# Optimization experiments

Measured on AMD Instinct MI355X. Metric: run time of the kernel, lower is better.

## Reference

```python
import jax, jax.numpy as jnp
import numpy as np
import math

D_MODEL = 1024
NHEAD = 16
D_HEAD = D_MODEL // NHEAD
B, S = 2, 2048


def setup_inputs() -> dict:
    key = jax.random.key(0)
    ks = jax.random.split(key, 8)
    scale = 1.0 / math.sqrt(D_MODEL)
    return {
        "q": jax.random.normal(ks[0], (B, S, D_MODEL), jnp.float32),
        "k": jax.random.normal(ks[1], (B, S, D_MODEL), jnp.float32),
        "v": jax.random.normal(ks[2], (B, S, D_MODEL), jnp.float32),
        "mask": jax.random.randint(ks[3], (B, S, S), 0, 2) == 1,
        "w_q": jax.random.normal(ks[4], (D_MODEL, D_MODEL), jnp.float32) * scale,
        "w_k": jax.random.normal(ks[5], (D_MODEL, D_MODEL), jnp.float32) * scale,
        "w_v": jax.random.normal(ks[6], (D_MODEL, D_MODEL), jnp.float32) * scale,
        "w_o": jax.random.normal(ks[7], (D_MODEL, D_MODEL), jnp.float32) * scale,
    }


def reference(q, k, v, mask, w_q, w_k, w_v, w_o):
    # Linear layers (torch Linear: x @ W.T), then the module's view(B, H, -1, d_head),
    # which is a plain reshape (sequence gets folded with heads), NOT a head-transpose.
    qh = (q @ w_q.T).reshape(B, NHEAD, -1, D_HEAD)  # (B,H,S,dh) via raw reshape
    kh = (k @ w_k.T).reshape(B, NHEAD, -1, D_HEAD)
    vh = (v @ w_v.T).reshape(B, NHEAD, -1, D_HEAD)

    u = jnp.einsum("bhqd,bhkd->bhqk", qh, kh) / math.sqrt(D_HEAD)  # (B,H,S,S)
    m = mask[:, None]  # (B,1,S,S)
    u = jnp.where(m, -jnp.inf, u)
    attn = jax.nn.softmax(u, axis=-1)
    attn = jnp.where(m, 0.0, attn)
    out = jnp.einsum("bhqk,bhkd->bhqd", attn, vh)  # (B,H,S,dh)
    out = out.reshape(B, -1, D_MODEL)  # raw reshape back, matching the module
    return out @ w_o.T
```

## Files before the change

kernel.cpp:

```cpp
#include <hip/hip_runtime.h>
#include <hip/hip_bf16.h>
#include <stdint.h>


typedef __attribute__((ext_vector_type(8))) short short8;
typedef __attribute__((ext_vector_type(4))) short s4v;
typedef __attribute__((ext_vector_type(4))) float floatx4;
using bf16 = __hip_bfloat16;

#define QSCALE 0.18033688011112042f

#define MFMA16(a, b, c) __builtin_amdgcn_mfma_f32_16x16x32_bf16(a, b, c, 0, 0, 0)

__device__ __forceinline__ void load_lds16(const bf16* g, bf16* l) {
  __builtin_amdgcn_global_load_lds(
      (const __attribute__((address_space(1))) void*)g,
      (__attribute__((address_space(3))) void*)l, 16, 0, 0);
}

__device__ __forceinline__ float scrub(float x) {
  return (x == x && fabsf(x) < 1e30f) ? x : 0.0f;
}

__device__ __forceinline__ int swz64(int row, int col) {
  return row * 64 + (col ^ ((row & 7) << 3));
}
__device__ __forceinline__ int swz128(int row, int col) {
  return row * 128 + (col ^ ((row & 15) << 3));
}

__global__ void k_detect(const uint16_t* __restrict__ q,
                         const uint16_t* __restrict__ mask,
                         int* __restrict__ flags) {
  __shared__ int f32, cat;
  const int tid = threadIdx.x;
  if (tid == 0) { f32 = 0; cat = 0; }
  __syncthreads();
  int hit = 0;
#pragma unroll
  for (int j = 0; j < 8; j++) {
    const short8 v8 = *(const short8*)(q + ((size_t)tid * 8 + j) * 8);
#pragma unroll
    for (int t = 0; t < 8; t++) {
      const int e = (((unsigned short)v8[t]) >> 7) & 0xFF;
      if (e == 0 || e == 0xFF) hit = 1;
    }
  }
  if (hit) atomicOr(&f32, 1);
  int c = 0;
  {
    const short8 m8 = *(const short8*)(mask + (size_t)tid * 8);
#pragma unroll
    for (int t = 0; t < 8; t++) {
      const uint32_t hw = (unsigned short)m8[t];
      const int i = tid * 8 + t;
      if (hw == 0x3C00u) c |= 4;
      else if (hw == 0x3F80u) c |= (i & 1) ? 2 : 1;
      else if (hw > 1u) c |= 8;
    }
  }
  if (c) atomicOr(&cat, c);
  __syncthreads();
  if (tid == 0) {
    flags[0] = f32;
    const int cc = cat;
    int mode;
    if (cc & 4)      mode = 2;
    else if (cc & 1) mode = 2;
    else if (cc & 2) mode = 3;
    else if (cc & 8) mode = 0;
    else             mode = 1;
    flags[1] = mode;
  }
}

__global__ __launch_bounds__(256) void k_prep(
    const void* __restrict__ qf, const void* __restrict__ kf,
    const void* __restrict__ vf, const void* __restrict__ wqf,
    const void* __restrict__ wkf, const void* __restrict__ wvf,
    const void* __restrict__ wof, const void* __restrict__ maskp,
    bf16* __restrict__ dst, uint32_t* __restrict__ bits,
    const int* __restrict__ flags, int conv) {
  const int f32 = flags[0];
  const size_t t0 = (size_t)blockIdx.x * 256 + threadIdx.x;
  const size_t nthr = (size_t)gridDim.x * 256;
  if (conv) {
    for (size_t c = t0; c < 2097152; c += nthr) {
      const size_t e = c * 8;
      const void* src; size_t off; float sc = 1.0f;
      if (e < 4194304)       { src = qf;  off = e;            sc = QSCALE; }
      else if (e < 8388608)  { src = kf;  off = e - 4194304;  }
      else if (e < 12582912) { src = vf;  off = e - 8388608;  }
      else if (e < 13631488) { src = wqf; off = e - 12582912; }
      else if (e < 14680064) { src = wkf; off = e - 13631488; }
      else if (e < 15728640) { src = wvf; off = e - 14680064; }
      else                   { src = wof; off = e - 15728640; }
      union { short8 v8; bf16 b[8]; } u;
      if (f32) {
        const float4* s4 = (const float4*)src + (off >> 2);
        const float4 f0 = s4[0];
        const float4 f1 = s4[1];
        u.b[0] = __float2bfloat16(f0.x * sc); u.b[1] = __float2bfloat16(f0.y * sc);
        u.b[2] = __float2bfloat16(f0.z * sc); u.b[3] = __float2bfloat16(f0.w * sc);
        u.b[4] = __float2bfloat16(f1.x * sc); u.b[5] = __float2bfloat16(f1.y * sc);
        u.b[6] = __float2bfloat16(f1.z * sc); u.b[7] = __float2bfloat16(f1.w * sc);
      } else {
        u.v8 = *(const short8*)((const bf16*)src + off);
        if (sc != 1.0f) {
#pragma unroll
          for (int j = 0; j < 8; j++)
            u.b[j] = __float2bfloat16(__bfloat162float(u.b[j]) * sc);
        }
      }
      *(short8*)(dst + e) = u.v8;
    }
  }
  const int mmode = flags[1];
  const int wid = (int)(t0 >> 6), ln = (int)(t0 & 63);
  const int nw = (int)(nthr >> 6);
  const int NG = 2 * 2048 * 2048 / 64;
  for (int g = wid; g < NG; g += nw) {
    const size_t e = (size_t)g * 64 + ln;
    bool v;
    if (mmode == 1)      v = ((const int*)maskp)[e] != 0;
    else if (mmode == 0) v = ((const uint8_t*)maskp)[e] != 0;
    else if (mmode == 2) v = ((const uint16_t*)maskp)[e] != 0;
    else                 v = ((const uint32_t*)maskp)[e] != 0;
    const unsigned long long m = __ballot(v);
    if (ln == 0)       bits[(size_t)g * 2]     = (uint32_t)m;
    else if (ln == 32) bits[(size_t)g * 2 + 1] = (uint32_t)(m >> 32);
  }
}

template <int ROWS>
__device__ __forceinline__ void stage_b16(const bf16* __restrict__ src,
                                          bf16* __restrict__ dst,
                                          int wv, int ln) {
#pragma unroll
  for (int i = 0; i < ROWS / 64; i++) {
    const int seg = i * 4 + wv;
    const int fb = seg * 1024 + ln * 16;
    const int row = fb >> 6, col = (fb & 63) >> 1;
    load_lds16(src + (size_t)row * 1024 + col, dst + seg * 512);
  }
}

__device__ __forceinline__ void stage_f32(const float* __restrict__ src,
                                          bf16* __restrict__ dst, int tid) {
#pragma unroll
  for (int it = 0; it < 2; ++it) {
    const int e0 = (it * 256 + tid) * 8;
    const int row = e0 >> 5, col = e0 & 31;
    const float* s = src + (size_t)row * 1024 + col;
    const float4 f0 = *(const float4*)s;
    const float4 f1 = *(const float4*)(s + 4);
    union { short8 v; bf16 b[8]; } u;
    u.b[0] = __float2bfloat16(f0.x); u.b[1] = __float2bfloat16(f0.y);
    u.b[2] = __float2bfloat16(f0.z); u.b[3] = __float2bfloat16(f0.w);
    u.b[4] = __float2bfloat16(f1.x); u.b[5] = __float2bfloat16(f1.y);
    u.b[6] = __float2bfloat16(f1.z); u.b[7] = __float2bfloat16(f1.w);
    *(short8*)(dst + e0) = u.v;
  }
}

template <int MT>
__device__ __forceinline__ void gemm_t(const void* __restrict__ A, int a_f32,
                                       const void* __restrict__ W, int w_f32,
                                       bf16* __restrict__ Out,
                                       float* __restrict__ OutF, int mode,
                                       float oscale) {
  constexpr int TI = MT / 32;
  __shared__ bf16 As[MT * 32];
  __shared__ bf16 Bs[128 * 32];
  const int tid = threadIdx.x;
  const int wv = tid >> 6, ln = tid & 63;
  const int m0 = blockIdx.x * MT, n0 = blockIdx.y * 128;
  const int wm = (wv >> 1) * (MT / 2), wn = (wv & 1) * 64;
  floatx4 acc[TI][4] = {};
  for (int k0 = 0; k0 < 1024; k0 += 32) {
    __syncthreads();
    if (MT == 128 && a_f32) stage_f32((const float*)A + (size_t)m0 * 1024 + k0, As, tid);
    else                    stage_b16<MT>((const bf16*)A + (size_t)m0 * 1024 + k0, As, wv, ln);
    if (w_f32) stage_f32((const float*)W + (size_t)n0 * 1024 + k0, Bs, tid);
    else       stage_b16<128>((const bf16*)W + (size_t)n0 * 1024 + k0, Bs, wv, ln);
    __syncthreads();
    const short* Ap = (const short*)As;
    const short* Bp = (const short*)Bs;
    short8 af[TI], bfr[4];
#pragma unroll
    for (int t = 0; t < TI; t++)
      af[t]  = *(const short8*)(Ap + (wm + t * 16 + (ln & 15)) * 32 + (ln >> 4) * 8);
#pragma unroll
    for (int t = 0; t < 4; t++)
      bfr[t] = *(const short8*)(Bp + (wn + t * 16 + (ln & 15)) * 32 + (ln >> 4) * 8);
#pragma unroll
    for (int ti = 0; ti < TI; ti++)
#pragma unroll
      for (int tj = 0; tj < 4; tj++)
        acc[ti][tj] = MFMA16(af[ti], bfr[tj], acc[ti][tj]);
  }
#pragma unroll
  for (int ti = 0; ti < TI; ti++)
#pragma unroll
    for (int tj = 0; tj < 4; tj++)
#pragma unroll
      for (int r = 0; r < 4; r++) {
        const int m = m0 + wm + ti * 16 + (ln >> 4) * 4 + r;
        const int n = n0 + wn + tj * 16 + (ln & 15);
        if (mode == 2) {
          OutF[(size_t)m * 1024 + n] = scrub(acc[ti][tj][r]);
        } else {
          const int b = m >> 11, s = m & 2047;
          const int h = s >> 7, sl = s & 127;
          const int oc = n >> 6, d = n & 63;
          const int t = sl * 16 + oc;
          size_t idx;
          if (mode == 0) idx = ((size_t)(b * 16 + h) * 2048 + t) * 64 + d;
          else           idx = ((size_t)(b * 16 + h) * 64 + d) * 2048 + t;
          Out[idx] = __float2bfloat16(scrub(acc[ti][tj][r]) * oscale);
        }
      }
}

__global__ __launch_bounds__(256, 2) void k_proj(
    const void* __restrict__ q, const void* __restrict__ k, const void* __restrict__ v,
    const void* __restrict__ wq, const void* __restrict__ wk, const void* __restrict__ wvv,
    bf16* __restrict__ QH, bf16* __restrict__ KH, bf16* __restrict__ VT,
    const int* __restrict__ flags, int conv) {
  const int z = blockIdx.z;
  const int fl = conv ? 0 : flags[0];
  const void* A = (z == 0) ? q : (z == 1) ? k : v;
  const void* W = (z == 0) ? wq : (z == 1) ? wk : wvv;
  bf16* O = (z == 0) ? QH : (z == 1) ? KH : VT;
  const float osc = (z == 0 && !conv) ? QSCALE : 1.0f;
  gemm_t<128>(A, fl, W, fl, O, nullptr, (z == 2) ? 1 : 0, osc);
}

__global__ __launch_bounds__(256, 2) void k_outp(
    const bf16* __restrict__ A, const void* __restrict__ W,
    float* __restrict__ Out, const int* __restrict__ flags, int conv) {
  const int wf = conv ? 0 : flags[0];
  gemm_t<64>(A, 0, W, wf, nullptr, Out, 2, 1.0f);
}

__global__ __launch_bounds__(512, 4) void k_attn(
    const bf16* __restrict__ QH, const bf16* __restrict__ KH,
    const bf16* __restrict__ VT, const uint32_t* __restrict__ bits,
    bf16* __restrict__ OB) {
  constexpr int S = 2048, D = 64;
  constexpr float NEGB = -60000.0f;
  __shared__ bf16 Ks[128 * 64];
  __shared__ bf16 Vs[64 * 128];
  __shared__ bf16 Ps[128 * 128];
  const int tid = threadIdx.x, wv = tid >> 6, ln = tid & 63;
  const int g = ln >> 4, lq = ln & 15;
  const int flat = blockIdx.y * gridDim.x + blockIdx.x;
  const int xcd = flat & 7, ii = flat >> 3;
  const int bh = (xcd << 2) | (ii >> 4);
  const int q0 = (ii & 15) * 128;
  const int b = bh >> 4, h = bh & 15;
  const int qrow = wv * 16;

  short8 qf[2];
#pragma unroll
  for (int kc = 0; kc < 2; kc++) {
    const int qr = q0 + qrow + lq;
    qf[kc] = *(const short8*)(QH + ((size_t)bh * S + qr) * D + kc * 32 + g * 8);
  }

  const bf16* Kbase = KH + (size_t)bh * S * D;
  const bf16* Vbase = VT + (size_t)bh * D * S;
  const uint32_t* Mb = bits + (size_t)b * 131072 + (size_t)(q0 + qrow + lq) * 64;
  short8 kreg[2], vreg[2];

#define LOAD_KV(kt_)                                                     \
  {                                                                      \
    const bf16* Kg = Kbase + (size_t)(kt_) * 128 * D;                    \
    const bf16* Vg = Vbase + (kt_) * 128;                                \
    _Pragma("unroll")                                                    \
    for (int i = 0; i < 2; i++) {                                        \
      const int seg = i * 8 + wv;                                        \
      const int e = seg * 512 + ln * 8;                                  \
      kreg[i] = *(const short8*)(Kg + e);                                \
      const int fb = (seg * 64 + ln) * 16;                               \
      const int dd = fb >> 8, cb = (fb & 255) >> 1;                      \
      vreg[i] = *(const short8*)(Vg + (size_t)dd * S + cb);              \
    }                                                                    \
  }

#define STORE_KV()                                                       \
  {                                                                      \
    _Pragma("unroll")                                                    \
    for (int i = 0; i < 2; i++) {                                        \
      const int seg = i * 8 + wv;                                        \
      const int e = seg * 512 + ln * 8;                                  \
      *(short8*)(Ks + swz64(e >> 6, e & 63)) = kreg[i];                  \
      const int fb = (seg * 64 + ln) * 16;                               \
      const int dd = fb >> 8, cb = (fb & 255) >> 1;                      \
      *(short8*)(Vs + swz128(dd, cb)) = vreg[i];                         \
    }                                                                    \
  }

  float lacc0 = 0.f, lacc1 = 0.f;
  floatx4 oacc[4] = {};

  LOAD_KV(0);
  uint4 mvn = *(const uint4*)(Mb + 0);
  STORE_KV();
  __syncthreads();

  for (int kt = 0; kt < 16; kt++) {
    const uint4 mv = mvn;
    if (kt < 15) {
      LOAD_KV(kt + 1);
      mvn = *(const uint4*)(Mb + (kt + 1) * 4);
    }

    floatx4 sc[8];
    {
      const short* Kp = (const short*)Ks;
      __builtin_amdgcn_s_setprio(1);
#pragma unroll
      for (int tj = 0; tj < 8; tj++) {
        const int krow = tj * 16 + lq;
        const int kcol = g * 8;
        const short8 k0f = *(const short8*)(Kp + swz64(krow, kcol));
        const short8 k1f = *(const short8*)(Kp + swz64(krow, 32 + kcol));
        floatx4 z = {0.f, 0.f, 0.f, 0.f};
        z = MFMA16(k0f, qf[0], z);
        z = MFMA16(k1f, qf[1], z);
        sc[tj] = z;
      }
      __builtin_amdgcn_s_setprio(0);
    }

    {
      const int prow = qrow + lq;
      const uint32_t mw4[4] = {mv.x, mv.y, mv.z, mv.w};
#pragma unroll
      for (int tj = 0; tj < 8; tj++) {
        const uint32_t nib = mw4[tj >> 1] >> (((tj & 1) << 4) + (g << 2));
        uint32_t pw0, pw1;
        {
          float p0, p1, p2, p3;
          const float u0 = (nib & 1u) ? NEGB : sc[tj][0];
          const float u1 = (nib & 2u) ? NEGB : sc[tj][1];
          const float u2 = (nib & 4u) ? NEGB : sc[tj][2];
          const float u3 = (nib & 8u) ? NEGB : sc[tj][3];
          asm("v_exp_f32 %0, %1" : "=v"(p0) : "v"(u0));
          asm("v_exp_f32 %0, %1" : "=v"(p1) : "v"(u1));
          asm("v_exp_f32 %0, %1" : "=v"(p2) : "v"(u2));
          asm("v_exp_f32 %0, %1" : "=v"(p3) : "v"(u3));
          lacc0 += p0 + p2;
          lacc1 += p1 + p3;
          asm("v_cvt_pk_bf16_f32 %0, %1, %2" : "=v"(pw0) : "v"(p0), "v"(p1));
          asm("v_cvt_pk_bf16_f32 %0, %1, %2" : "=v"(pw1) : "v"(p2), "v"(p3));
        }
        uint2 pu; pu.x = pw0; pu.y = pw1;
        *(uint2*)(Ps + swz128(prow, tj * 16 + g * 4)) = pu;
      }
    }

    {
      const short* Pp = (const short*)Ps;
      const short* Vp = (const short*)Vs;
      __builtin_amdgcn_s_setprio(1);
#pragma unroll
      for (int kc = 0; kc < 4; kc++) {
        const short8 ap = *(const short8*)(Pp + swz128(qrow + lq, kc * 32 + g * 8));
#pragma unroll
        for (int tj = 0; tj < 4; tj++) {
          const short8 bv = *(const short8*)(Vp + swz128(tj * 16 + lq, kc * 32 + g * 8));
          oacc[tj] = MFMA16(ap, bv, oacc[tj]);
        }
      }
      __builtin_amdgcn_s_setprio(0);
    }
    __syncthreads();
    if (kt < 15) STORE_KV();
    __syncthreads();
  }

  {
    float s2 = lacc0 + lacc1;
    s2 += __shfl_xor(s2, 16);
    s2 += __shfl_xor(s2, 32);
    const float rlq = (s2 > 1e-35f) ? 1.f / s2 : 0.f;
    bf16* row = Ps + wv * 2048;
#pragma unroll
    for (int r = 0; r < 4; r++) {
      const float rl = __shfl(rlq, (ln & 48) | ((g << 2) + r), 64);
#pragma unroll
      for (int tj = 0; tj < 4; tj++) {
        row[(g * 4 + r) * 64 + tj * 16 + lq] =
            __float2bfloat16(scrub(oacc[tj][r] * rl));
      }
    }
    __builtin_amdgcn_s_waitcnt(0);
    const int s = h * 128 + ((q0 + qrow) >> 4);
    bf16* Og = OB + ((size_t)b * S + s) * 1024;
#pragma unroll
    for (int c = 0; c < 2; c++)
      *(short8*)(Og + c * 512 + ln * 8) = *(const short8*)(row + c * 512 + ln * 8);
  }
#undef LOAD_KV
#undef STORE_KV
}

extern "C" void kernel_launch(void* const* d_in, const int* in_sizes, int n_in,
                              void* d_out, int out_size, void* d_ws, size_t ws_size,
                              hipStream_t stream) {
  const void* q  = d_in[0];
  const void* k  = d_in[1];
  const void* v  = d_in[2];
  const void* mask = d_in[3];
  const void* wq = d_in[4];
  const void* wk = d_in[5];
  const void* wv = d_in[6];
  const void* wo = d_in[7];
  float* out = (float*)d_out;

  char* ws = (char*)d_ws;
  int* flags = (int*)ws;
  bf16* QH = (bf16*)(ws + 256);
  bf16* KH = QH + 4194304;
  bf16* VT = KH + 4194304;
  uint32_t* bits = (uint32_t*)(VT + 4194304);
  bf16* CV = (bf16*)(ws + 256 + 3 * 8388608 + 1048576);

  const size_t NEED = 256 + 3 * 8388608 + 1048576 + 33554432;
  const int conv = (ws_size >= NEED) ? 1 : 0;

  k_detect<<<1, 256, 0, stream>>>((const uint16_t*)q, (const uint16_t*)mask, flags);
  k_prep<<<2048, 256, 0, stream>>>(q, k, v, wq, wk, wv, wo, mask, CV, bits,
                                   flags, conv);

  const void *pq = q, *pk = k, *pv = v, *pwq = wq, *pwk = wk, *pwv = wv, *pwo = wo;
  if (conv) {
    pq  = CV;             pk  = CV + 4194304;  pv  = CV + 8388608;
    pwq = CV + 12582912;  pwk = CV + 13631488; pwv = CV + 14680064;
    pwo = CV + 15728640;
  }

  k_proj<<<dim3(32, 8, 3), 256, 0, stream>>>(pq, pk, pv, pwq, pwk, pwv,
                                             QH, KH, VT, flags, conv);
  k_attn<<<dim3(16, 32), 512, 0, stream>>>(QH, KH, VT, bits, QH );
  k_outp<<<dim3(64, 8), 256, 0, stream>>>(QH, pwo, out, flags, conv);
}
```

Measured before the change: 268.4 us.

## Widen GEMM K-tile to 64 with swizzled LDS and fold dtype detection into prep

The projection GEMM now stages K-chunks of 64 instead of 32, which halves the number of barrier-separated iterations. Both the bf16 global-to-LDS path and the fp32 staging path write through an XOR swizzle to avoid LDS bank conflicts on fragment reads. Each prep block now detects the input dtype and mask format itself, so the separate single-block detect kernel only launches when conversion is off. In exchange, LDS use doubles per block, which may lower occupancy, and every prep block repeats the small detection read.

```diff
diff --git a/kernel.cpp b/kernel.cpp
--- a/kernel.cpp
+++ b/kernel.cpp
@@ -79,10 +79,48 @@
     const void* __restrict__ vf, const void* __restrict__ wqf,
     const void* __restrict__ wkf, const void* __restrict__ wvf,
     const void* __restrict__ wof, const void* __restrict__ maskp,
-    bf16* __restrict__ dst, uint32_t* __restrict__ bits,
-    const int* __restrict__ flags, int conv) {
-  const int f32 = flags[0];
-  const size_t t0 = (size_t)blockIdx.x * 256 + threadIdx.x;
+    bf16* __restrict__ dst, uint32_t* __restrict__ bits, int conv) {
+  __shared__ int sf32, scat;
+  const int tid = threadIdx.x;
+  if (tid == 0) { sf32 = 0; scat = 0; }
+  __syncthreads();
+  {
+    int hit = 0;
+    const uint16_t* qh = (const uint16_t*)qf;
+#pragma unroll
+    for (int j = 0; j < 8; j++) {
+      const short8 v8 = *(const short8*)(qh + ((size_t)tid * 8 + j) * 8);
+#pragma unroll
+      for (int t = 0; t < 8; t++) {
+        const int e = (((unsigned short)v8[t]) >> 7) & 0xFF;
+        if (e == 0 || e == 0xFF) hit = 1;
+      }
+    }
+    if (hit) atomicOr(&sf32, 1);
+    int c = 0;
+    const short8 m8 = *(const short8*)((const uint16_t*)maskp + (size_t)tid * 8);
+#pragma unroll
+    for (int t = 0; t < 8; t++) {
+      const uint32_t hw = (unsigned short)m8[t];
+      const int i = tid * 8 + t;
+      if (hw == 0x3C00u) c |= 4;
+      else if (hw == 0x3F80u) c |= (i & 1) ? 2 : 1;
+      else if (hw > 1u) c |= 8;
+    }
+    if (c) atomicOr(&scat, c);
+  }
+  __syncthreads();
+  const int f32 = sf32;
+  int mmode;
+  {
+    const int cc = scat;
+    if (cc & 4)      mmode = 2;
+    else if (cc & 1) mmode = 2;
+    else if (cc & 2) mmode = 3;
+    else if (cc & 8) mmode = 0;
+    else             mmode = 1;
+  }
+  const size_t t0 = (size_t)blockIdx.x * 256 + tid;
   const size_t nthr = (size_t)gridDim.x * 256;
   if (conv) {
     for (size_t c = t0; c < 2097152; c += nthr) {
@@ -115,7 +153,6 @@
       *(short8*)(dst + e) = u.v8;
     }
   }
-  const int mmode = flags[1];
   const int wid = (int)(t0 >> 6), ln = (int)(t0 & 63);
   const int nw = (int)(nthr >> 6);
   const int NG = 2 * 2048 * 2048 / 64;
@@ -137,20 +174,22 @@
                                           bf16* __restrict__ dst,
                                           int wv, int ln) {
 #pragma unroll
-  for (int i = 0; i < ROWS / 64; i++) {
+  for (int i = 0; i < ROWS / 32; i++) {
     const int seg = i * 4 + wv;
-    const int fb = seg * 1024 + ln * 16;
-    const int row = fb >> 6, col = (fb & 63) >> 1;
-    load_lds16(src + (size_t)row * 1024 + col, dst + seg * 512);
-  }
-}
-
+    const int row = seg * 8 + (ln >> 3);
+    const int ch = ln & 7;
+    load_lds16(src + (size_t)row * 1024 + ((ch ^ (row & 7)) << 3),
+               dst + seg * 512);
+  }
+}
+
+template <int ROWS>
 __device__ __forceinline__ void stage_f32(const float* __restrict__ src,
                                           bf16* __restrict__ dst, int tid) {
 #pragma unroll
-  for (int it = 0; it < 2; ++it) {
+  for (int it = 0; it < ROWS / 32; ++it) {
     const int e0 = (it * 256 + tid) * 8;
-    const int row = e0 >> 5, col = e0 & 31;
+    const int row = e0 >> 6, col = e0 & 63;
     const float* s = src + (size_t)row * 1024 + col;
     const float4 f0 = *(const float4*)s;
     const float4 f1 = *(const float4*)(s + 4);
@@ -159,7 +198,7 @@
     u.b[2] = __float2bfloat16(f0.z); u.b[3] = __float2bfloat16(f0.w);
     u.b[4] = __float2bfloat16(f1.x); u.b[5] = __float2bfloat16(f1.y);
     u.b[6] = __float2bfloat16(f1.z); u.b[7] = __float2bfloat16(f1.w);
-    *(short8*)(dst + e0) = u.v;
+    *(short8*)(dst + swz64(row, col)) = u.v;
   }
 }
 
@@ -170,34 +209,41 @@
                                        float* __restrict__ OutF, int mode,
                                        float oscale) {
   constexpr int TI = MT / 32;
-  __shared__ bf16 As[MT * 32];
-  __shared__ bf16 Bs[128 * 32];
+  __shared__ bf16 As[MT * 64];
+  __shared__ bf16 Bs[128 * 64];
   const int tid = threadIdx.x;
   const int wv = tid >> 6, ln = tid & 63;
+  const int g = ln >> 4;
   const int m0 = blockIdx.x * MT, n0 = blockIdx.y * 128;
   const int wm = (wv >> 1) * (MT / 2), wn = (wv & 1) * 64;
   floatx4 acc[TI][4] = {};
-  for (int k0 = 0; k0 < 1024; k0 += 32) {
+  for (int k0 = 0; k0 < 1024; k0 += 64) {
     __syncthreads();
-    if (MT == 128 && a_f32) stage_f32((const float*)A + (size_t)m0 * 1024 + k0, As, tid);
-    else                    stage_b16<MT>((const bf16*)A + (size_t)m0 * 1024 + k0, As, wv, ln);
-    if (w_f32) stage_f32((const float*)W + (size_t)n0 * 1024 + k0, Bs, tid);
+    if (a_f32) stage_f32<MT>((const float*)A + (size_t)m0 * 1024 + k0, As, tid);
+    else       stage_b16<MT>((const bf16*)A + (size_t)m0 * 1024 + k0, As, wv, ln);
+    if (w_f32) stage_f32<128>((const float*)W + (size_t)n0 * 1024 + k0, Bs, tid);
     else       stage_b16<128>((const bf16*)W + (size_t)n0 * 1024 + k0, Bs, wv, ln);
     __syncthreads();
     const short* Ap = (const short*)As;
     const short* Bp = (const short*)Bs;
-    short8 af[TI], bfr[4];
+    short8 af[TI][2], bfr[4][2];
 #pragma unroll
     for (int t = 0; t < TI; t++)
-      af[t]  = *(const short8*)(Ap + (wm + t * 16 + (ln & 15)) * 32 + (ln >> 4) * 8);
+#pragma unroll
+      for (int kc = 0; kc < 2; kc++)
+        af[t][kc] = *(const short8*)(Ap + swz64(wm + t * 16 + (ln & 15), kc * 32 + g * 8));
 #pragma unroll
     for (int t = 0; t < 4; t++)
-      bfr[t] = *(const short8*)(Bp + (wn + t * 16 + (ln & 15)) * 32 + (ln >> 4) * 8);
-#pragma unroll
-    for (int ti = 0; ti < TI; ti++)
-#pragma unroll
-      for (int tj = 0; tj < 4; tj++)
-        acc[ti][tj] = MFMA16(af[ti], bfr[tj], acc[ti][tj]);
+#pragma unroll
+      for (int kc = 0; kc < 2; kc++)
+        bfr[t][kc] = *(const short8*)(Bp + swz64(wn + t * 16 + (ln & 15), kc * 32 + g * 8));
+#pragma unroll
+    for (int kc = 0; kc < 2; kc++)
+#pragma unroll
+      for (int ti = 0; ti < TI; ti++)
+#pragma unroll
+        for (int tj = 0; tj < 4; tj++)
+          acc[ti][tj] = MFMA16(af[ti][kc], bfr[tj][kc], acc[ti][tj]);
   }
 #pragma unroll
   for (int ti = 0; ti < TI; ti++)
@@ -431,9 +477,9 @@
   const size_t NEED = 256 + 3 * 8388608 + 1048576 + 33554432;
   const int conv = (ws_size >= NEED) ? 1 : 0;
 
-  k_detect<<<1, 256, 0, stream>>>((const uint16_t*)q, (const uint16_t*)mask, flags);
-  k_prep<<<2048, 256, 0, stream>>>(q, k, v, wq, wk, wv, wo, mask, CV, bits,
-                                   flags, conv);
+  k_prep<<<2048, 256, 0, stream>>>(q, k, v, wq, wk, wv, wo, mask, CV, bits, conv);
+  if (!conv)
+    k_detect<<<1, 256, 0, stream>>>((const uint16_t*)q, (const uint16_t*)mask, flags);
 
   const void *pq = q, *pk = k, *pv = v, *pwq = wq, *pwk = wk, *pwv = wv, *pwo = wo;
   if (conv) {
```

Result: no change. 264.2 us (-1.6%).
